# Kernel optimization log

Measured on AMD Instinct MI355X. Metric: run time of the kernel, lower is better.

## Reference

```python
import jax, jax.numpy as jnp
import numpy as np

B, C, H, W = 16, 256, 128, 128
K = 7
EPS = 1e-5


def conv2d(x, w, pad):
    # x [B,Ci,H,W], w [Co,Ci,kh,kw] -> NCHW conv, stride 1
    return jax.lax.conv_general_dilated(
        x, w, window_strides=(1, 1), padding=[(pad, pad), (pad, pad)],
        dimension_numbers=("NCHW", "OIHW", "NCHW"))


def grid_sample_bilinear(feat, grid):
    """torch.F.grid_sample(mode='bilinear', padding_mode='zeros', align_corners=False).
    feat [B,C,H,W], grid [B,H,W,2] with (x,y) in [-1,1]. Returns [B,C,H,W]."""
    b, c, h, w = feat.shape
    ix = ((grid[..., 0] + 1.0) * w - 1.0) * 0.5  # unnormalize, align_corners=False
    iy = ((grid[..., 1] + 1.0) * h - 1.0) * 0.5
    x0 = jnp.floor(ix)
    y0 = jnp.floor(iy)
    x1 = x0 + 1.0
    y1 = y0 + 1.0
    wx1 = ix - x0
    wx0 = 1.0 - wx1
    wy1 = iy - y0
    wy0 = 1.0 - wy1
    feat_flat = feat.reshape(b, c, h * w)

    def gather(xi, yi):
        xi_i = xi.astype(jnp.int32)
        yi_i = yi.astype(jnp.int32)
        valid = ((xi_i >= 0) & (xi_i < w) & (yi_i >= 0) & (yi_i < h)).astype(feat.dtype)
        xc = jnp.clip(xi_i, 0, w - 1)
        yc = jnp.clip(yi_i, 0, h - 1)
        idx = (yc * w + xc).reshape(b, 1, h * w)
        vals = jnp.take_along_axis(feat_flat, jnp.broadcast_to(idx, (b, c, h * w)), axis=2)
        return vals.reshape(b, c, h, w) * valid[:, None]

    out = (gather(x0, y0) * (wx0 * wy0)[:, None]
           + gather(x1, y0) * (wx1 * wy0)[:, None]
           + gather(x0, y1) * (wx0 * wy1)[:, None]
           + gather(x1, y1) * (wx1 * wy1)[:, None])
    return out


def setup_inputs() -> dict:
    key = jax.random.key(0)
    ks = jax.random.split(key, 5)
    return {
        "x": jax.random.normal(ks[0], (B, C, H, W), jnp.float32),
        "w1": jax.random.normal(ks[1], (16, 2, 3, 3), jnp.float32) * 0.1,
        "bn_gamma": jnp.ones((16,), jnp.float32),
        "bn_beta": jnp.zeros((16,), jnp.float32),
        "bn_mean": jnp.zeros((16,), jnp.float32),
        "bn_var": jnp.ones((16,), jnp.float32),
        "w2": jax.random.normal(ks[2], (2 * K * K, 16, 3, 3), jnp.float32) * 0.05,
        "b2": jax.random.normal(ks[3], (2 * K * K,), jnp.float32) * 0.05,
        "attn_w": jax.random.normal(ks[4], (1, 2, K, K), jnp.float32) * 0.1,
    }


def reference(x, w1, bn_gamma, bn_beta, bn_mean, bn_var, w2, b2, attn_w):
    # CBAM-style spatial descriptor
    avg = jnp.mean(x, axis=1, keepdims=True)
    mx = jnp.max(x, axis=1, keepdims=True)
    sf = jnp.concatenate([avg, mx], axis=1)  # [B,2,H,W]

    # offset branch: conv3x3 -> BN(eval) -> ReLU -> conv3x3(+bias)
    h1 = conv2d(sf, w1, 1)
    scale = (bn_gamma * jax.lax.rsqrt(bn_var + EPS))[None, :, None, None]
    h1 = jax.nn.relu((h1 - bn_mean[None, :, None, None]) * scale + bn_beta[None, :, None, None])
    off = conv2d(h1, w2, 1) + b2[None, :, None, None]  # [B,2*K*K,H,W]

    b_, _, h_, w_ = off.shape
    off = off.reshape(b_, 2, K * K, h_, w_).mean(axis=2)  # [B,2,H,W]
    off = jnp.tanh(off) * 0.5
    off = jnp.transpose(off, (0, 2, 3, 1))  # [B,H,W,2]

    gy, gx = jnp.meshgrid(jnp.linspace(-1.0, 1.0, h_, dtype=sf.dtype),
                          jnp.linspace(-1.0, 1.0, w_, dtype=sf.dtype), indexing="ij")
    base = jnp.stack([gx, gy], axis=-1)[None]  # [1,H,W,2]
    grid = jnp.clip(base + off, -1.0, 1.0)

    sampled = grid_sample_bilinear(sf, grid)  # [B,2,H,W]
    attn = conv2d(sampled, attn_w, K // 2)  # [B,1,H,W]
    return jax.nn.sigmoid(attn)
```

## Files before the change

kernel.cpp:

```cpp
#include <hip/hip_runtime.h>
#include <math.h>

#define B_  16
#define C_  256
#define H_  128
#define W_  128
#define HW  16384
#define KK  7

__global__ __launch_bounds__(512) void k_stage1(const float* __restrict__ x,
                                                const float* __restrict__ w2,
                                                const float* __restrict__ b2,
                                                float* __restrict__ sf,
                                                float* __restrict__ w2r,
                                                float* __restrict__ b2r) {
    if (blockIdx.x == 256) {
        int tid = threadIdx.x;
        if (tid < 288) {
            int c = tid / 144;
            int r = tid % 144;
            float s = 0.f;
            for (int j = 0; j < 49; ++j) s += w2[(size_t)(c * 49 + j) * 144 + r];
            w2r[tid] = s * (1.0f / 49.0f);
        } else if (tid < 290) {
            int c = tid - 288;
            float s = 0.f;
            for (int j = 0; j < 49; ++j) s += b2[c * 49 + j];
            b2r[c] = s * (1.0f / 49.0f);
        }
        return;
    }

    __shared__ float4 ls[256];
    __shared__ float4 lm[256];

    int tid  = threadIdx.x;
    int lane = tid & 255;
    int half = tid >> 8;
    int pos  = blockIdx.x * 256 + lane;
    int b    = pos >> 12;
    int p    = pos & 4095;

    const float4* xp = (const float4*)x
                     + (size_t)b * (C_ * 4096)
                     + (size_t)(half * 128) * 4096
                     + p;

    float4 s0 = make_float4(0.f, 0.f, 0.f, 0.f), s1 = s0, s2 = s0, s3 = s0;
    const float NI = -3.402823466e+38f;
    float4 m0 = make_float4(NI, NI, NI, NI), m1 = m0, m2 = m0, m3 = m0;

    for (int c = 0; c < 128; c += 8) {
        float4 v0 = xp[(size_t)(c + 0) * 4096];
        float4 v1 = xp[(size_t)(c + 1) * 4096];
        float4 v2 = xp[(size_t)(c + 2) * 4096];
        float4 v3 = xp[(size_t)(c + 3) * 4096];
        float4 v4 = xp[(size_t)(c + 4) * 4096];
        float4 v5 = xp[(size_t)(c + 5) * 4096];
        float4 v6 = xp[(size_t)(c + 6) * 4096];
        float4 v7 = xp[(size_t)(c + 7) * 4096];

        s0.x += v0.x; s0.y += v0.y; s0.z += v0.z; s0.w += v0.w;
        s1.x += v1.x; s1.y += v1.y; s1.z += v1.z; s1.w += v1.w;
        s2.x += v2.x; s2.y += v2.y; s2.z += v2.z; s2.w += v2.w;
        s3.x += v3.x; s3.y += v3.y; s3.z += v3.z; s3.w += v3.w;
        s0.x += v4.x; s0.y += v4.y; s0.z += v4.z; s0.w += v4.w;
        s1.x += v5.x; s1.y += v5.y; s1.z += v5.z; s1.w += v5.w;
        s2.x += v6.x; s2.y += v6.y; s2.z += v6.z; s2.w += v6.w;
        s3.x += v7.x; s3.y += v7.y; s3.z += v7.z; s3.w += v7.w;

        m0.x = fmaxf(m0.x, v0.x); m0.y = fmaxf(m0.y, v0.y); m0.z = fmaxf(m0.z, v0.z); m0.w = fmaxf(m0.w, v0.w);
        m1.x = fmaxf(m1.x, v1.x); m1.y = fmaxf(m1.y, v1.y); m1.z = fmaxf(m1.z, v1.z); m1.w = fmaxf(m1.w, v1.w);
        m2.x = fmaxf(m2.x, v2.x); m2.y = fmaxf(m2.y, v2.y); m2.z = fmaxf(m2.z, v2.z); m2.w = fmaxf(m2.w, v2.w);
        m3.x = fmaxf(m3.x, v3.x); m3.y = fmaxf(m3.y, v3.y); m3.z = fmaxf(m3.z, v3.z); m3.w = fmaxf(m3.w, v3.w);
        m0.x = fmaxf(m0.x, v4.x); m0.y = fmaxf(m0.y, v4.y); m0.z = fmaxf(m0.z, v4.z); m0.w = fmaxf(m0.w, v4.w);
        m1.x = fmaxf(m1.x, v5.x); m1.y = fmaxf(m1.y, v5.y); m1.z = fmaxf(m1.z, v5.z); m1.w = fmaxf(m1.w, v5.w);
        m2.x = fmaxf(m2.x, v6.x); m2.y = fmaxf(m2.y, v6.y); m2.z = fmaxf(m2.z, v6.z); m2.w = fmaxf(m2.w, v6.w);
        m3.x = fmaxf(m3.x, v7.x); m3.y = fmaxf(m3.y, v7.y); m3.z = fmaxf(m3.z, v7.z); m3.w = fmaxf(m3.w, v7.w);
    }

    float4 s, m;
    s.x = (s0.x + s1.x) + (s2.x + s3.x);
    s.y = (s0.y + s1.y) + (s2.y + s3.y);
    s.z = (s0.z + s1.z) + (s2.z + s3.z);
    s.w = (s0.w + s1.w) + (s2.w + s3.w);
    m.x = fmaxf(fmaxf(m0.x, m1.x), fmaxf(m2.x, m3.x));
    m.y = fmaxf(fmaxf(m0.y, m1.y), fmaxf(m2.y, m3.y));
    m.z = fmaxf(fmaxf(m0.z, m1.z), fmaxf(m2.z, m3.z));
    m.w = fmaxf(fmaxf(m0.w, m1.w), fmaxf(m2.w, m3.w));

    if (half == 1) { ls[lane] = s; lm[lane] = m; }
    __syncthreads();
    if (half == 0) {
        float4 s2_ = ls[lane];
        float4 m2_ = lm[lane];
        const float inv = 1.0f / 256.0f;
        s.x = (s.x + s2_.x) * inv; s.y = (s.y + s2_.y) * inv;
        s.z = (s.z + s2_.z) * inv; s.w = (s.w + s2_.w) * inv;
        m.x = fmaxf(m.x, m2_.x); m.y = fmaxf(m.y, m2_.y);
        m.z = fmaxf(m.z, m2_.z); m.w = fmaxf(m.w, m2_.w);

        float4* o = (float4*)sf;
        o[(size_t)b * 8192 + p]        = s;
        o[(size_t)b * 8192 + 4096 + p] = m;
    }
}

__global__ __launch_bounds__(256) void k_off_sample(const float* __restrict__ sf,
                                                    const float* __restrict__ w1,
                                                    const float* __restrict__ gamma,
                                                    const float* __restrict__ beta,
                                                    const float* __restrict__ mean,
                                                    const float* __restrict__ var,
                                                    const float* __restrict__ w2r,
                                                    const float* __restrict__ b2r,
                                                    float* __restrict__ sampled) {
    __shared__ float sft[2][20][20];
    __shared__ float h1t[16][18][18];
    __shared__ float wl1[288], wl2[288];
    __shared__ float sc[16], bi[16], bl[2];

    int tid = threadIdx.x;
    for (int i = tid; i < 288; i += 256) { wl1[i] = w1[i]; wl2[i] = w2r[i]; }
    if (tid < 16) {
        float s = gamma[tid] * rsqrtf(var[tid] + 1e-5f);
        sc[tid] = s;
        bi[tid] = beta[tid] - mean[tid] * s;
    }
    if (tid < 2) bl[tid] = b2r[tid];

    int blk = blockIdx.x;
    int b   = blk >> 6;
    int t8  = blk & 63;
    int ty0 = (t8 >> 3) << 4;
    int tx0 = (t8 & 7) << 4;
    const float* sfb = sf + ((size_t)b << 15);

    for (int i = tid; i < 400; i += 256) {
        int ly = i / 20, lx = i % 20;
        int gy = ty0 + ly - 2, gx = tx0 + lx - 2;
        bool ok = (gy >= 0) & (gy < H_) & (gx >= 0) & (gx < W_);
        int gidx = gy * W_ + gx;
        sft[0][ly][lx] = ok ? sfb[gidx]      : 0.f;
        sft[1][ly][lx] = ok ? sfb[HW + gidx] : 0.f;
    }
    __syncthreads();

    for (int i = tid; i < 324; i += 256) {
        int ly = i / 18, lx = i % 18;
        int gy = ty0 + ly - 1, gx = tx0 + lx - 1;
        bool inside = (gy >= 0) & (gy < H_) & (gx >= 0) & (gx < W_);
        float in[2][9];
#pragma unroll
        for (int c = 0; c < 2; ++c)
#pragma unroll
            for (int kh = 0; kh < 3; ++kh)
#pragma unroll
                for (int kw = 0; kw < 3; ++kw)
                    in[c][kh * 3 + kw] = sft[c][ly + kh][lx + kw];
#pragma unroll
        for (int oc = 0; oc < 16; ++oc) {
            float acc = 0.f;
#pragma unroll
            for (int c = 0; c < 2; ++c)
#pragma unroll
                for (int k = 0; k < 9; ++k)
                    acc += in[c][k] * wl1[oc * 18 + c * 9 + k];
            h1t[oc][ly][lx] = inside ? fmaxf(acc * sc[oc] + bi[oc], 0.f) : 0.f;
        }
    }
    __syncthreads();

    int ly = tid >> 4, lx = tid & 15;
    float off0 = bl[0], off1 = bl[1];
#pragma unroll 4
    for (int ci = 0; ci < 16; ++ci) {
#pragma unroll
        for (int kh = 0; kh < 3; ++kh)
#pragma unroll
            for (int kw = 0; kw < 3; ++kw) {
                float v = h1t[ci][ly + kh][lx + kw];
                off0 += v * wl2[ci * 9 + kh * 3 + kw];
                off1 += v * wl2[144 + ci * 9 + kh * 3 + kw];
            }
    }
    off0 = tanhf(off0) * 0.5f;
    off1 = tanhf(off1) * 0.5f;

    int h = ty0 + ly, w = tx0 + lx;
    float gx = fmaf((float)w, 2.0f / 127.0f, -1.0f) + off0;
    float gy = fmaf((float)h, 2.0f / 127.0f, -1.0f) + off1;
    gx = fminf(fmaxf(gx, -1.0f), 1.0f);
    gy = fminf(fmaxf(gy, -1.0f), 1.0f);

    float ix = (gx + 1.0f) * 64.0f - 0.5f;
    float iy = (gy + 1.0f) * 64.0f - 0.5f;
    float x0f = floorf(ix), y0f = floorf(iy);
    int x0 = (int)x0f, y0 = (int)y0f;
    int x1 = x0 + 1,  y1 = y0 + 1;
    float wx1 = ix - x0f, wx0 = 1.0f - wx1;
    float wy1 = iy - y0f, wy0 = 1.0f - wy1;

    float o0 = 0.f, o1 = 0.f;
    if (x0 >= 0 && x0 < W_ && y0 >= 0 && y0 < H_) {
        int idx = y0 * W_ + x0; float wt = wx0 * wy0;
        o0 += sfb[idx] * wt; o1 += sfb[HW + idx] * wt;
    }
    if (x1 >= 0 && x1 < W_ && y0 >= 0 && y0 < H_) {
        int idx = y0 * W_ + x1; float wt = wx1 * wy0;
        o0 += sfb[idx] * wt; o1 += sfb[HW + idx] * wt;
    }
    if (x0 >= 0 && x0 < W_ && y1 >= 0 && y1 < H_) {
        int idx = y1 * W_ + x0; float wt = wx0 * wy1;
        o0 += sfb[idx] * wt; o1 += sfb[HW + idx] * wt;
    }
    if (x1 >= 0 && x1 < W_ && y1 >= 0 && y1 < H_) {
        int idx = y1 * W_ + x1; float wt = wx1 * wy1;
        o0 += sfb[idx] * wt; o1 += sfb[HW + idx] * wt;
    }
    int hw = h * W_ + w;
    sampled[((size_t)b << 15) + hw]      = o0;
    sampled[((size_t)b << 15) + HW + hw] = o1;
}

__global__ __launch_bounds__(256) void k_attn(const float* __restrict__ sampled,
                                              const float* __restrict__ aw,
                                              float* __restrict__ out) {
    __shared__ float tile[2][22][22];
    __shared__ float wl[98];
    int tid = threadIdx.x;
    if (tid < 98) wl[tid] = aw[tid];

    int blk = blockIdx.x;
    int b   = blk >> 6;
    int t8  = blk & 63;
    int ty0 = (t8 >> 3) << 4;
    int tx0 = (t8 & 7) << 4;
    const float* sb = sampled + ((size_t)b << 15);

    for (int i = tid; i < 484; i += 256) {
        int ly = i / 22, lx = i % 22;
        int gy = ty0 + ly - 3, gx = tx0 + lx - 3;
        bool ok = (gy >= 0) & (gy < H_) & (gx >= 0) & (gx < W_);
        int gidx = gy * W_ + gx;
        tile[0][ly][lx] = ok ? sb[gidx]      : 0.f;
        tile[1][ly][lx] = ok ? sb[HW + gidx] : 0.f;
    }
    __syncthreads();

    int ly = tid >> 4, lx = tid & 15;
    float acc = 0.f;
#pragma unroll
    for (int c = 0; c < 2; ++c)
#pragma unroll
        for (int ky = 0; ky < KK; ++ky)
#pragma unroll
            for (int kx = 0; kx < KK; ++kx)
                acc += tile[c][ly + ky][lx + kx] * wl[c * 49 + ky * 7 + kx];

    int h = ty0 + ly, w = tx0 + lx;
    out[((size_t)b << 14) + h * W_ + w] = 1.0f / (1.0f + expf(-acc));
}

extern "C" void kernel_launch(void* const* d_in, const int* in_sizes, int n_in,
                              void* d_out, int out_size, void* d_ws, size_t ws_size,
                              hipStream_t stream) {
    const float* x     = (const float*)d_in[0];
    const float* w1    = (const float*)d_in[1];
    const float* bn_g  = (const float*)d_in[2];
    const float* bn_b  = (const float*)d_in[3];
    const float* bn_m  = (const float*)d_in[4];
    const float* bn_v  = (const float*)d_in[5];
    const float* w2    = (const float*)d_in[6];
    const float* b2    = (const float*)d_in[7];
    const float* aw    = (const float*)d_in[8];
    float* out = (float*)d_out;

    float* ws = (float*)d_ws;
    float* sf      = ws;
    float* sampled = sf + (size_t)B_ * 2 * HW;
    float* w2r     = sampled + (size_t)B_ * 2 * HW;
    float* b2r     = w2r + 288;

    k_stage1<<<257, 512, 0, stream>>>(x, w2, b2, sf, w2r, b2r);
    k_off_sample<<<B_ * 64, 256, 0, stream>>>(sf, w1, bn_g, bn_b, bn_m, bn_v,
                                              w2r, b2r, sampled);
    k_attn<<<B_ * 64, 256, 0, stream>>>(sampled, aw, out);
}
```

Baseline: 412.2 us.

## Fuse offset/sampling kernel with 7x7 attention conv using halo recompute

Merges the offset+grid-sample kernel with the attention convolution kernel. Each tile now computes sampled values on a 22x22 halo region in shared memory (with larger sf and h1 halos) and applies the 7x7 conv directly. This removes the intermediate sampled buffer round trip and one launch, at the cost of recomputing the offset branch and bilinear sampling on overlapping halos.

```diff
diff --git a/kernel.cpp b/kernel.cpp
--- a/kernel.cpp
+++ b/kernel.cpp
@@ -106,22 +106,25 @@
     }
 }
 
-__global__ __launch_bounds__(256) void k_off_sample(const float* __restrict__ sf,
-                                                    const float* __restrict__ w1,
-                                                    const float* __restrict__ gamma,
-                                                    const float* __restrict__ beta,
-                                                    const float* __restrict__ mean,
-                                                    const float* __restrict__ var,
-                                                    const float* __restrict__ w2r,
-                                                    const float* __restrict__ b2r,
-                                                    float* __restrict__ sampled) {
-    __shared__ float sft[2][20][20];
-    __shared__ float h1t[16][18][18];
-    __shared__ float wl1[288], wl2[288];
+__global__ __launch_bounds__(256) void k_off_attn(const float* __restrict__ sf,
+                                                  const float* __restrict__ w1,
+                                                  const float* __restrict__ gamma,
+                                                  const float* __restrict__ beta,
+                                                  const float* __restrict__ mean,
+                                                  const float* __restrict__ var,
+                                                  const float* __restrict__ w2r,
+                                                  const float* __restrict__ b2r,
+                                                  const float* __restrict__ aw,
+                                                  float* __restrict__ out) {
+    __shared__ float sft[2][26][26];
+    __shared__ float h1t[16][24][24];
+    __shared__ float smp[2][22][22];
+    __shared__ float wl1[288], wl2[288], wl4[98];
     __shared__ float sc[16], bi[16], bl[2];
 
     int tid = threadIdx.x;
     for (int i = tid; i < 288; i += 256) { wl1[i] = w1[i]; wl2[i] = w2r[i]; }
+    if (tid < 98) wl4[tid] = aw[tid];
     if (tid < 16) {
         float s = gamma[tid] * rsqrtf(var[tid] + 1e-5f);
         sc[tid] = s;
@@ -136,9 +139,9 @@
     int tx0 = (t8 & 7) << 4;
     const float* sfb = sf + ((size_t)b << 15);
 
-    for (int i = tid; i < 400; i += 256) {
-        int ly = i / 20, lx = i % 20;
-        int gy = ty0 + ly - 2, gx = tx0 + lx - 2;
+    for (int i = tid; i < 676; i += 256) {
+        int ly = i / 26, lx = i % 26;
+        int gy = ty0 + ly - 5, gx = tx0 + lx - 5;
         bool ok = (gy >= 0) & (gy < H_) & (gx >= 0) & (gx < W_);
         int gidx = gy * W_ + gx;
         sft[0][ly][lx] = ok ? sfb[gidx]      : 0.f;
@@ -146,9 +149,9 @@
     }
     __syncthreads();
 
-    for (int i = tid; i < 324; i += 256) {
-        int ly = i / 18, lx = i % 18;
-        int gy = ty0 + ly - 1, gx = tx0 + lx - 1;
+    for (int i = tid; i < 576; i += 256) {
+        int ly = i / 24, lx = i % 24;
+        int gy = ty0 + ly - 4, gx = tx0 + lx - 4;
         bool inside = (gy >= 0) & (gy < H_) & (gx >= 0) & (gx < W_);
         float in[2][9];
 #pragma unroll
@@ -171,80 +174,58 @@
     }
     __syncthreads();
 
-    int ly = tid >> 4, lx = tid & 15;
-    float off0 = bl[0], off1 = bl[1];
-#pragma unroll 4
-    for (int ci = 0; ci < 16; ++ci) {
-#pragma unroll
-        for (int kh = 0; kh < 3; ++kh)
-#pragma unroll
-            for (int kw = 0; kw < 3; ++kw) {
-                float v = h1t[ci][ly + kh][lx + kw];
-                off0 += v * wl2[ci * 9 + kh * 3 + kw];
-                off1 += v * wl2[144 + ci * 9 + kh * 3 + kw];
-            }
-    }
-    off0 = tanhf(off0) * 0.5f;
-    off1 = tanhf(off1) * 0.5f;
-
-    int h = ty0 + ly, w = tx0 + lx;
-    float gx = fmaf((float)w, 2.0f / 127.0f, -1.0f) + off0;
-    float gy = fmaf((float)h, 2.0f / 127.0f, -1.0f) + off1;
-    gx = fminf(fmaxf(gx, -1.0f), 1.0f);
-    gy = fminf(fmaxf(gy, -1.0f), 1.0f);
-
-    float ix = (gx + 1.0f) * 64.0f - 0.5f;
-    float iy = (gy + 1.0f) * 64.0f - 0.5f;
-    float x0f = floorf(ix), y0f = floorf(iy);
-    int x0 = (int)x0f, y0 = (int)y0f;
-    int x1 = x0 + 1,  y1 = y0 + 1;
-    float wx1 = ix - x0f, wx0 = 1.0f - wx1;
-    float wy1 = iy - y0f, wy0 = 1.0f - wy1;
-
-    float o0 = 0.f, o1 = 0.f;
-    if (x0 >= 0 && x0 < W_ && y0 >= 0 && y0 < H_) {
-        int idx = y0 * W_ + x0; float wt = wx0 * wy0;
-        o0 += sfb[idx] * wt; o1 += sfb[HW + idx] * wt;
-    }
-    if (x1 >= 0 && x1 < W_ && y0 >= 0 && y0 < H_) {
-        int idx = y0 * W_ + x1; float wt = wx1 * wy0;
-        o0 += sfb[idx] * wt; o1 += sfb[HW + idx] * wt;
-    }
-    if (x0 >= 0 && x0 < W_ && y1 >= 0 && y1 < H_) {
-        int idx = y1 * W_ + x0; float wt = wx0 * wy1;
-        o0 += sfb[idx] * wt; o1 += sfb[HW + idx] * wt;
-    }
-    if (x1 >= 0 && x1 < W_ && y1 >= 0 && y1 < H_) {
-        int idx = y1 * W_ + x1; float wt = wx1 * wy1;
-        o0 += sfb[idx] * wt; o1 += sfb[HW + idx] * wt;
-    }
-    int hw = h * W_ + w;
-    sampled[((size_t)b << 15) + hw]      = o0;
-    sampled[((size_t)b << 15) + HW + hw] = o1;
-}
-
-__global__ __launch_bounds__(256) void k_attn(const float* __restrict__ sampled,
-                                              const float* __restrict__ aw,
-                                              float* __restrict__ out) {
-    __shared__ float tile[2][22][22];
-    __shared__ float wl[98];
-    int tid = threadIdx.x;
-    if (tid < 98) wl[tid] = aw[tid];
-
-    int blk = blockIdx.x;
-    int b   = blk >> 6;
-    int t8  = blk & 63;
-    int ty0 = (t8 >> 3) << 4;
-    int tx0 = (t8 & 7) << 4;
-    const float* sb = sampled + ((size_t)b << 15);
-
     for (int i = tid; i < 484; i += 256) {
         int ly = i / 22, lx = i % 22;
-        int gy = ty0 + ly - 3, gx = tx0 + lx - 3;
-        bool ok = (gy >= 0) & (gy < H_) & (gx >= 0) & (gx < W_);
-        int gidx = gy * W_ + gx;
-        tile[0][ly][lx] = ok ? sb[gidx]      : 0.f;
-        tile[1][ly][lx] = ok ? sb[HW + gidx] : 0.f;
+        int h = ty0 + ly - 3, w = tx0 + lx - 3;
+        bool inside = (h >= 0) & (h < H_) & (w >= 0) & (w < W_);
+
+        float off0 = bl[0], off1 = bl[1];
+#pragma unroll 4
+        for (int ci = 0; ci < 16; ++ci) {
+#pragma unroll
+            for (int kh = 0; kh < 3; ++kh)
+#pragma unroll
+                for (int kw = 0; kw < 3; ++kw) {
+                    float v = h1t[ci][ly + kh][lx + kw];
+                    off0 += v * wl2[ci * 9 + kh * 3 + kw];
+                    off1 += v * wl2[144 + ci * 9 + kh * 3 + kw];
+                }
+        }
+        off0 = tanhf(off0) * 0.5f;
+        off1 = tanhf(off1) * 0.5f;
+
+        float gx = fmaf((float)w, 2.0f / 127.0f, -1.0f) + off0;
+        float gy = fmaf((float)h, 2.0f / 127.0f, -1.0f) + off1;
+        gx = fminf(fmaxf(gx, -1.0f), 1.0f);
+        gy = fminf(fmaxf(gy, -1.0f), 1.0f);
+
+        float ix = (gx + 1.0f) * 64.0f - 0.5f;
+        float iy = (gy + 1.0f) * 64.0f - 0.5f;
+        float x0f = floorf(ix), y0f = floorf(iy);
+        int x0 = (int)x0f, y0 = (int)y0f;
+        int x1 = x0 + 1,  y1 = y0 + 1;
+        float wx1 = ix - x0f, wx0 = 1.0f - wx1;
+        float wy1 = iy - y0f, wy0 = 1.0f - wy1;
+
+        float o0 = 0.f, o1 = 0.f;
+        if (x0 >= 0 && x0 < W_ && y0 >= 0 && y0 < H_) {
+            int idx = y0 * W_ + x0; float wt = wx0 * wy0;
+            o0 += sfb[idx] * wt; o1 += sfb[HW + idx] * wt;
+        }
+        if (x1 >= 0 && x1 < W_ && y0 >= 0 && y0 < H_) {
+            int idx = y0 * W_ + x1; float wt = wx1 * wy0;
+            o0 += sfb[idx] * wt; o1 += sfb[HW + idx] * wt;
+        }
+        if (x0 >= 0 && x0 < W_ && y1 >= 0 && y1 < H_) {
+            int idx = y1 * W_ + x0; float wt = wx0 * wy1;
+            o0 += sfb[idx] * wt; o1 += sfb[HW + idx] * wt;
+        }
+        if (x1 >= 0 && x1 < W_ && y1 >= 0 && y1 < H_) {
+            int idx = y1 * W_ + x1; float wt = wx1 * wy1;
+            o0 += sfb[idx] * wt; o1 += sfb[HW + idx] * wt;
+        }
+        smp[0][ly][lx] = inside ? o0 : 0.f;
+        smp[1][ly][lx] = inside ? o1 : 0.f;
     }
     __syncthreads();
 
@@ -256,7 +237,7 @@
         for (int ky = 0; ky < KK; ++ky)
 #pragma unroll
             for (int kx = 0; kx < KK; ++kx)
-                acc += tile[c][ly + ky][lx + kx] * wl[c * 49 + ky * 7 + kx];
+                acc += smp[c][ly + ky][lx + kx] * wl4[c * 49 + ky * 7 + kx];
 
     int h = ty0 + ly, w = tx0 + lx;
     out[((size_t)b << 14) + h * W_ + w] = 1.0f / (1.0f + expf(-acc));
@@ -277,13 +258,11 @@
     float* out = (float*)d_out;
 
     float* ws = (float*)d_ws;
-    float* sf      = ws;
-    float* sampled = sf + (size_t)B_ * 2 * HW;
-    float* w2r     = sampled + (size_t)B_ * 2 * HW;
-    float* b2r     = w2r + 288;
+    float* sf  = ws;
+    float* w2r = sf + (size_t)B_ * 2 * HW;
+    float* b2r = w2r + 288;
 
     k_stage1<<<257, 512, 0, stream>>>(x, w2, b2, sf, w2r, b2r);
-    k_off_sample<<<B_ * 64, 256, 0, stream>>>(sf, w1, bn_g, bn_b, bn_m, bn_v,
-                                              w2r, b2r, sampled);
-    k_attn<<<B_ * 64, 256, 0, stream>>>(sampled, aw, out);
+    k_off_attn<<<B_ * 64, 256, 0, stream>>>(sf, w1, bn_g, bn_b, bn_m, bn_v,
+                                            w2r, b2r, aw, out);
 }
```

After: 429.4 us. 4.2% more time.
